# Optimization experiments

Measured on AMD Instinct MI355X. Metric: run time of the kernel, lower is better.

Reference implementation:

```python
import jax, jax.numpy as jnp
import numpy as np

B, D, E, K = 8192, 768, 8, 32  # batch, hidden, n_main_intents, max sub-intents


def setup_inputs() -> dict:
    key = jax.random.key(0)
    k1, k2, k3, k4, k5 = jax.random.split(key, 5)
    pooled = jax.random.normal(k1, (B, D), dtype=jnp.float32)
    main_W = jax.random.normal(k2, (D, E), dtype=jnp.float32) * 0.02
    main_b = jax.random.normal(k3, (E,), dtype=jnp.float32) * 0.02
    sub_W = jax.random.normal(k4, (E, D, K), dtype=jnp.float32) * 0.02
    sub_b = jax.random.normal(k5, (E, K), dtype=jnp.float32) * 0.02
    # sub-classifier output sizes per main intent: 32,31,...,25 (from intent_structure)
    sub_sizes = (K - jnp.arange(E)).astype(jnp.int32)
    return {"pooled": pooled, "main_W": main_W, "main_b": main_b,
            "sub_W": sub_W, "sub_b": sub_b, "sub_sizes": sub_sizes}


def reference(pooled, main_W, main_b, sub_W, sub_b, sub_sizes):
    # Dropout(0.3) is identity in eval mode.
    main_out = pooled @ main_W + main_b                      # [B, E]
    idx = jnp.argmax(main_out, axis=1)                       # top-1 routing [B]
    Wg = jnp.take(sub_W, idx, axis=0)                        # gather [B, D, K]
    bg = jnp.take(sub_b, idx, axis=0)                        # [B, K]
    sub_out = jnp.einsum('bd,bdk->bk', pooled, Wg) + bg      # per-sample small GEMV
    # padded scatter: sub_outputs[i, :n_sub(idx_i)] = sub_out, rest stays zero
    valid = jnp.arange(K)[None, :] < jnp.take(sub_sizes, idx)[:, None]
    sub_out = jnp.where(valid, sub_out, jnp.zeros((), sub_out.dtype))
    return main_out, sub_out
```

## Files before the change

### kernel.cpp

```cpp
#include <hip/hip_runtime.h>

#define BB 8192
#define DD 768
#define EE 8
#define KK 32
#define BM 32
#define NBLK (BB / BM)
#define NSTEP (DD / 32)

typedef short    short8 __attribute__((ext_vector_type(8)));
typedef float    f32x4  __attribute__((ext_vector_type(4)));
typedef float    f32x8  __attribute__((ext_vector_type(8)));
typedef unsigned short us4 __attribute__((ext_vector_type(4)));

__device__ __forceinline__ unsigned short f2bf(float f) {
  unsigned int u = __float_as_uint(f);
  u = (u + 0x7fffu + ((u >> 16) & 1u)) >> 16;
  return (unsigned short)u;
}

__global__ __launch_bounds__(256) void pack_w(const float* __restrict__ sw,
                                              short* __restrict__ bp) {
  const int t    = blockIdx.x * 256 + threadIdx.x;
  const int lane = t & 63;
  const int half = (t >> 6) & 1;
  const int s    = (t >> 7) % NSTEP;
  const int e    = (t >> 7) / NSTEP;
  const int lc   = lane & 15, hi = lane >> 4;
  const int k    = half * 16 + lc;
  const int d0   = s * 32 + hi * 8;
  const float* src = sw + ((size_t)(e * DD + d0)) * KK + k;
  short8 v;
#pragma unroll
  for (int j = 0; j < 8; ++j) v[j] = (short)f2bf(src[(size_t)j * KK]);
  *(short8*)(bp + (size_t)t * 8) = v;
}

__global__ __launch_bounds__(512) void fused(
    const float* __restrict__ pooled, const float* __restrict__ mW,
    const float* __restrict__ mb, const short* __restrict__ Bp,
    const float* __restrict__ sub_b, const int* __restrict__ sub_sizes,
    float* __restrict__ main_out, float* __restrict__ sub_out) {
  __shared__ short aS[BM][776];
  __shared__ int   idxS[BM];
  __shared__ int   szS[BM];

  const int t    = threadIdx.x;
  const int w    = t >> 6;
  const int lane = t & 63;
  const int row0 = blockIdx.x * BM;

  f32x8 acc[4] = {};
#pragma unroll 1
  for (int i = 0; i < 3; ++i) {
    const int d = (i * 64 + lane) * 4;
    f32x8 W0 = *(const f32x8*)(mW + (size_t)(d + 0) * EE);
    f32x8 W1 = *(const f32x8*)(mW + (size_t)(d + 1) * EE);
    f32x8 W2 = *(const f32x8*)(mW + (size_t)(d + 2) * EE);
    f32x8 W3 = *(const f32x8*)(mW + (size_t)(d + 3) * EE);
#pragma unroll
    for (int rr = 0; rr < 4; ++rr) {
      const int r = w * 4 + rr;
      f32x4 v = *(const f32x4*)(pooled + (size_t)(row0 + r) * DD + d);
      us4 u;
      u[0] = f2bf(v[0]); u[1] = f2bf(v[1]); u[2] = f2bf(v[2]); u[3] = f2bf(v[3]);
      *(us4*)&aS[r][d] = u;
      acc[rr] += v[0] * W0;
      acc[rr] += v[1] * W1;
      acc[rr] += v[2] * W2;
      acc[rr] += v[3] * W3;
    }
  }
#pragma unroll
  for (int rr = 0; rr < 4; ++rr) {
#pragma unroll
    for (int off = 32; off >= 1; off >>= 1) {
#pragma unroll
      for (int j = 0; j < 8; ++j) acc[rr][j] += __shfl_xor(acc[rr][j], off);
    }
    if (lane == 0) {
      const int r = w * 4 + rr;
      f32x8 res = acc[rr] + *(const f32x8*)mb;
      *(f32x8*)(main_out + (size_t)(row0 + r) * EE) = res;
      float best = res[0];
      int   bi   = 0;
#pragma unroll
      for (int e = 1; e < EE; ++e) {
        if (res[e] > best) { best = res[e]; bi = e; }
      }
      idxS[r] = bi;
      szS[r]  = sub_sizes[bi];
    }
  }
  __syncthreads();

  const int lc = lane & 15, hi = lane >> 4;
  const short* bpw = Bp + (size_t)w * (NSTEP * 1024) + (size_t)lane * 8;
  f32x4 c[2][2] = {};

#pragma unroll 4
  for (int s = 0; s < NSTEP; ++s) {
    short8 b0 = *(const short8*)(bpw + s * 1024);
    short8 b1 = *(const short8*)(bpw + s * 1024 + 512);
    const int dd = s * 32 + hi * 8;
    short8 a0 = *(const short8*)&aS[lc][dd];
    short8 a1 = *(const short8*)&aS[16 + lc][dd];
    c[0][0] = __builtin_amdgcn_mfma_f32_16x16x32_bf16(a0, b0, c[0][0], 0, 0, 0);
    c[0][1] = __builtin_amdgcn_mfma_f32_16x16x32_bf16(a0, b1, c[0][1], 0, 0, 0);
    c[1][0] = __builtin_amdgcn_mfma_f32_16x16x32_bf16(a1, b0, c[1][0], 0, 0, 0);
    c[1][1] = __builtin_amdgcn_mfma_f32_16x16x32_bf16(a1, b1, c[1][1], 0, 0, 0);
  }

#pragma unroll
  for (int n = 0; n < 2; ++n) {
    const int k = n * 16 + lc;
    const float bias = sub_b[w * KK + k];
#pragma unroll
    for (int mt = 0; mt < 2; ++mt) {
#pragma unroll
      for (int q = 0; q < 4; ++q) {
        const int rl = mt * 16 + hi * 4 + q;
        if (idxS[rl] == w) {
          float v = c[mt][n][q] + bias;
          if (k >= szS[rl]) v = 0.f;
          sub_out[(size_t)(row0 + rl) * KK + k] = v;
        }
      }
    }
  }
}

extern "C" void kernel_launch(void* const* d_in, const int* in_sizes, int n_in,
                              void* d_out, int out_size, void* d_ws, size_t ws_size,
                              hipStream_t stream) {
  const float* pooled   = (const float*)d_in[0];
  const float* main_W   = (const float*)d_in[1];
  const float* main_b   = (const float*)d_in[2];
  const float* sub_W    = (const float*)d_in[3];
  const float* sub_b    = (const float*)d_in[4];
  const int*   sub_size = (const int*)d_in[5];

  float* main_out = (float*)d_out;
  float* sub_out  = (float*)d_out + (size_t)BB * EE;
  short* Bp       = (short*)d_ws;

  pack_w<<<96, 256, 0, stream>>>(sub_W, Bp);
  fused<<<NBLK, 512, 0, stream>>>(pooled, main_W, main_b, Bp, sub_b,
                                  sub_size, main_out, sub_out);
}
```

Before: 29.74 us.

## Prefetch packed sub-weights before main GEMV and split pack_w work finer

Loads the first eight K-steps of packed bf16 sub-classifier weights into registers at kernel start, so their global latency overlaps the main-intent GEMV and routing phase. The first eight MFMA steps are then peeled off and use the prefetched registers. The pack kernel now has each thread write four bf16 values instead of eight, doubling its grid for more parallelism. The fused kernel also gets a launch-bounds occupancy hint of two blocks. The prefetch costs extra registers (16 short8 values per lane), which may limit occupancy.

```diff
diff --git a/kernel.cpp b/kernel.cpp
--- a/kernel.cpp
+++ b/kernel.cpp
@@ -7,7 +7,9 @@
 #define BM 32
 #define NBLK (BB / BM)
 #define NSTEP (DD / 32)
+#define PF 8
 
+typedef short    short4s __attribute__((ext_vector_type(4)));
 typedef short    short8 __attribute__((ext_vector_type(8)));
 typedef float    f32x4  __attribute__((ext_vector_type(4)));
 typedef float    f32x8  __attribute__((ext_vector_type(8)));
@@ -22,21 +24,23 @@
 __global__ __launch_bounds__(256) void pack_w(const float* __restrict__ sw,
                                               short* __restrict__ bp) {
   const int t    = blockIdx.x * 256 + threadIdx.x;
-  const int lane = t & 63;
-  const int half = (t >> 6) & 1;
-  const int s    = (t >> 7) % NSTEP;
-  const int e    = (t >> 7) / NSTEP;
+  const int h    = t & 1;
+  const int f    = t >> 1;
+  const int lane = f & 63;
+  const int half = (f >> 6) & 1;
+  const int s    = (f >> 7) % NSTEP;
+  const int e    = (f >> 7) / NSTEP;
   const int lc   = lane & 15, hi = lane >> 4;
   const int k    = half * 16 + lc;
-  const int d0   = s * 32 + hi * 8;
+  const int d0   = s * 32 + hi * 8 + h * 4;
   const float* src = sw + ((size_t)(e * DD + d0)) * KK + k;
-  short8 v;
+  short4s v;
 #pragma unroll
-  for (int j = 0; j < 8; ++j) v[j] = (short)f2bf(src[(size_t)j * KK]);
-  *(short8*)(bp + (size_t)t * 8) = v;
+  for (int j = 0; j < 4; ++j) v[j] = (short)f2bf(src[(size_t)j * KK]);
+  *(short4s*)(bp + (size_t)t * 4) = v;
 }
 
-__global__ __launch_bounds__(512) void fused(
+__global__ __launch_bounds__(512, 2) void fused(
     const float* __restrict__ pooled, const float* __restrict__ mW,
     const float* __restrict__ mb, const short* __restrict__ Bp,
     const float* __restrict__ sub_b, const int* __restrict__ sub_sizes,
@@ -49,6 +53,15 @@
   const int w    = t >> 6;
   const int lane = t & 63;
   const int row0 = blockIdx.x * BM;
+  const int lc   = lane & 15, hi = lane >> 4;
+
+  const short* bpw = Bp + (size_t)w * (NSTEP * 1024) + (size_t)lane * 8;
+  short8 bpre0[PF], bpre1[PF];
+#pragma unroll
+  for (int s = 0; s < PF; ++s) {
+    bpre0[s] = *(const short8*)(bpw + s * 1024);
+    bpre1[s] = *(const short8*)(bpw + s * 1024 + 512);
+  }
 
   f32x8 acc[4] = {};
 #pragma unroll 1
@@ -94,12 +107,21 @@
   }
   __syncthreads();
 
-  const int lc = lane & 15, hi = lane >> 4;
-  const short* bpw = Bp + (size_t)w * (NSTEP * 1024) + (size_t)lane * 8;
   f32x4 c[2][2] = {};
 
+#pragma unroll
+  for (int s = 0; s < PF; ++s) {
+    const int dd = s * 32 + hi * 8;
+    short8 a0 = *(const short8*)&aS[lc][dd];
+    short8 a1 = *(const short8*)&aS[16 + lc][dd];
+    c[0][0] = __builtin_amdgcn_mfma_f32_16x16x32_bf16(a0, bpre0[s], c[0][0], 0, 0, 0);
+    c[0][1] = __builtin_amdgcn_mfma_f32_16x16x32_bf16(a0, bpre1[s], c[0][1], 0, 0, 0);
+    c[1][0] = __builtin_amdgcn_mfma_f32_16x16x32_bf16(a1, bpre0[s], c[1][0], 0, 0, 0);
+    c[1][1] = __builtin_amdgcn_mfma_f32_16x16x32_bf16(a1, bpre1[s], c[1][1], 0, 0, 0);
+  }
+
 #pragma unroll 4
-  for (int s = 0; s < NSTEP; ++s) {
+  for (int s = PF; s < NSTEP; ++s) {
     short8 b0 = *(const short8*)(bpw + s * 1024);
     short8 b1 = *(const short8*)(bpw + s * 1024 + 512);
     const int dd = s * 32 + hi * 8;
@@ -144,7 +166,7 @@
   float* sub_out  = (float*)d_out + (size_t)BB * EE;
   short* Bp       = (short*)d_ws;
 
-  pack_w<<<96, 256, 0, stream>>>(sub_W, Bp);
+  pack_w<<<192, 256, 0, stream>>>(sub_W, Bp);
   fused<<<NBLK, 512, 0, stream>>>(pooled, main_W, main_b, Bp, sub_b,
                                   sub_size, main_out, sub_out);
 }
```

New measurement: 29.84 us. Within noise of the previous version (+0.3%).

## Fuse weight packing into main kernel via cooperative grid sync

Applied to the files above, without the earlier changes.

The separate pack_w launch that converts sub_W to bf16 MFMA layout is removed. Its work now runs at the start of the fused kernel, spread across all 256 blocks with half-size work items, followed by a threadfence and a cooperative grid-wide sync. This drops one kernel launch and the gap between launches, at the cost of a grid barrier that every block must wait on and the constraints of a cooperative launch.

```diff
diff --git a/kernel.cpp b/kernel.cpp
--- a/kernel.cpp
+++ b/kernel.cpp
@@ -1,4 +1,7 @@
 #include <hip/hip_runtime.h>
+#include <hip/hip_cooperative_groups.h>
+
+namespace cg = cooperative_groups;
 
 #define BB 8192
 #define DD 768
@@ -8,6 +11,7 @@
 #define NBLK (BB / BM)
 #define NSTEP (DD / 32)
 
+typedef short    short4s __attribute__((ext_vector_type(4)));
 typedef short    short8 __attribute__((ext_vector_type(8)));
 typedef float    f32x4  __attribute__((ext_vector_type(4)));
 typedef float    f32x8  __attribute__((ext_vector_type(8)));
@@ -19,27 +23,11 @@
   return (unsigned short)u;
 }
 
-__global__ __launch_bounds__(256) void pack_w(const float* __restrict__ sw,
-                                              short* __restrict__ bp) {
-  const int t    = blockIdx.x * 256 + threadIdx.x;
-  const int lane = t & 63;
-  const int half = (t >> 6) & 1;
-  const int s    = (t >> 7) % NSTEP;
-  const int e    = (t >> 7) / NSTEP;
-  const int lc   = lane & 15, hi = lane >> 4;
-  const int k    = half * 16 + lc;
-  const int d0   = s * 32 + hi * 8;
-  const float* src = sw + ((size_t)(e * DD + d0)) * KK + k;
-  short8 v;
-#pragma unroll
-  for (int j = 0; j < 8; ++j) v[j] = (short)f2bf(src[(size_t)j * KK]);
-  *(short8*)(bp + (size_t)t * 8) = v;
-}
-
 __global__ __launch_bounds__(512) void fused(
     const float* __restrict__ pooled, const float* __restrict__ mW,
-    const float* __restrict__ mb, const short* __restrict__ Bp,
-    const float* __restrict__ sub_b, const int* __restrict__ sub_sizes,
+    const float* __restrict__ mb, const float* __restrict__ sub_W,
+    short* __restrict__ Bp, const float* __restrict__ sub_b,
+    const int* __restrict__ sub_sizes,
     float* __restrict__ main_out, float* __restrict__ sub_out) {
   __shared__ short aS[BM][776];
   __shared__ int   idxS[BM];
@@ -49,6 +37,29 @@
   const int w    = t >> 6;
   const int lane = t & 63;
   const int row0 = blockIdx.x * BM;
+  const int lc   = lane & 15, hi = lane >> 4;
+
+  {
+    const int g = blockIdx.x * 512 + t;
+    if (g < 2 * EE * NSTEP * 128) {
+      const int h    = g & 1;
+      const int f    = g >> 1;
+      const int pl   = f & 63;
+      const int half = (f >> 6) & 1;
+      const int s    = (f >> 7) % NSTEP;
+      const int e    = (f >> 7) / NSTEP;
+      const int plc  = pl & 15, phi = pl >> 4;
+      const int k    = half * 16 + plc;
+      const int d0   = s * 32 + phi * 8 + h * 4;
+      const float* src = sub_W + ((size_t)(e * DD + d0)) * KK + k;
+      short4s v;
+#pragma unroll
+      for (int j = 0; j < 4; ++j) v[j] = (short)f2bf(src[(size_t)j * KK]);
+      *(short4s*)(Bp + (size_t)g * 4) = v;
+    }
+  }
+  __threadfence();
+  cg::this_grid().sync();
 
   f32x8 acc[4] = {};
 #pragma unroll 1
@@ -94,7 +105,6 @@
   }
   __syncthreads();
 
-  const int lc = lane & 15, hi = lane >> 4;
   const short* bpw = Bp + (size_t)w * (NSTEP * 1024) + (size_t)lane * 8;
   f32x4 c[2][2] = {};
 
@@ -144,7 +154,9 @@
   float* sub_out  = (float*)d_out + (size_t)BB * EE;
   short* Bp       = (short*)d_ws;
 
-  pack_w<<<96, 256, 0, stream>>>(sub_W, Bp);
-  fused<<<NBLK, 512, 0, stream>>>(pooled, main_W, main_b, Bp, sub_b,
-                                  sub_size, main_out, sub_out);
+  void* args[] = {(void*)&pooled, (void*)&main_W, (void*)&main_b,
+                  (void*)&sub_W,  (void*)&Bp,     (void*)&sub_b,
+                  (void*)&sub_size, (void*)&main_out, (void*)&sub_out};
+  hipLaunchCooperativeKernel((void*)fused, dim3(NBLK), dim3(512), args, 0,
+                             stream);
 }
```

Measured after the change: 91.93 us. +209.1%, slower.
